# Kernel tuning notes

Hardware: AMD Instinct MI355X
Metric: run time of the kernel (lower is better)

Reference implementation:

```python
import jax, jax.numpy as jnp
import numpy as np

B_, C_, H_, W_, N_ = 2, 256, 64, 64, 16


def setup_inputs() -> dict:
    key = jax.random.key(0)
    ks = jax.random.split(key, 6)
    return {
        "features": jax.random.normal(ks[0], (B_, C_, H_, W_), jnp.float32),
        "A_log": jax.random.normal(ks[1], (C_, N_), jnp.float32) * 0.5,
        "D": jax.random.normal(ks[2], (C_,), jnp.float32),
        "W_delta": jax.random.normal(ks[3], (C_, C_), jnp.float32) * 0.02,
        "b_delta": jnp.zeros((C_,), jnp.float32),
        "W_B": jax.random.normal(ks[4], (C_, N_), jnp.float32) * 0.02,
        "W_C": jax.random.normal(ks[5], (C_, N_), jnp.float32) * 0.02,
    }


def _selective_scan(x, A_log, D, W_delta, b_delta, W_B, W_C):
    # x: (B, L, C) -> (B, L, C). Canonical S6 selective scan (mamba corrector).
    delta = jax.nn.softplus(x @ W_delta + b_delta)          # (B, L, C)
    Bm = x @ W_B                                            # (B, L, N)
    Cm = x @ W_C                                            # (B, L, N)
    A = -jnp.exp(A_log)                                     # (C, N), negative real
    dA = jnp.exp(delta[..., None] * A)                      # (B, L, C, N)
    dBx = (delta * x)[..., None] * Bm[:, :, None, :]        # (B, L, C, N)

    def combine(left, right):
        a_l, b_l = left
        a_r, b_r = right
        return (a_l * a_r, a_r * b_l + b_r)

    # h_t = dA_t * h_{t-1} + dBx_t, computed in parallel over L
    _, h = jax.lax.associative_scan(combine, (dA, dBx), axis=1)
    y = jnp.einsum('blcn,bln->blc', h, Cm) + x * D          # (B, L, C)
    return y


def reference(features, A_log, D, W_delta, b_delta, W_B, W_C):
    B, C, H, W = features.shape
    corr = lambda x: _selective_scan(x, A_log, D, W_delta, b_delta, W_B, W_C)

    # direction 1: row-major forward
    flat = features.reshape(B, C, H * W).transpose(0, 2, 1)        # (B, HW, C)
    out1 = corr(flat)
    # direction 2: row-major reversed
    out2 = jnp.flip(corr(jnp.flip(flat, axis=1)), axis=1)
    # direction 3: rows flipped vertically (flip over H), scan, flip back
    rows = features.transpose(0, 2, 3, 1)                          # (B, H, W, C)
    rows_f = jnp.flip(rows, axis=1).reshape(B, H * W, C)
    out3 = jnp.flip(corr(rows_f).reshape(B, H, W, C), axis=1).reshape(B, H * W, C)
    # direction 4: column-major, flipped over W, scan, flip + transpose back
    cols = features.transpose(0, 3, 2, 1)                          # (B, W, H, C)
    cols_f = jnp.flip(cols, axis=1).reshape(B, W * H, C)
    out4 = jnp.flip(corr(cols_f).reshape(B, W, H, C), axis=1)
    out4 = out4.transpose(0, 2, 1, 3).reshape(B, H * W, C)

    mamba_out = (out1 + out2 + out3 + out4) / 4                    # (B, HW, C)
    return mamba_out.transpose(0, 2, 1).reshape(B, C, H, W)
```

## Files before the change

### kernel.cpp

```cpp
#include <hip/hip_runtime.h>
#include <cstdint>
#include <cstddef>

#define BB 2
#define CC 256
#define NN 16
#define LL 4096
#define NCH 128
#define CLEN 32
#define LCH 16
#define LOG2E 1.4426950408889634f

__device__ __forceinline__ float softplus_f(float z) {
    return fmaxf(z, 0.f) + log1pf(expf(-fabsf(z)));
}

__global__ __launch_bounds__(256) void k1_delta_gemm(
    const float* __restrict__ feat, const float* __restrict__ Wd,
    const float* __restrict__ bd, const float* __restrict__ WB,
    const float* __restrict__ WC, float* __restrict__ du,
    float* __restrict__ Bm, float* __restrict__ Cm)
{
    int lc = blockIdx.x & 255;
    int b  = blockIdx.x >> 8;
    int l0 = lc * LCH;
    int c  = threadIdx.x;
    const float* fbase = feat + (size_t)b * CC * LL;

    int lB  = threadIdx.x >> 4;
    int s   = threadIdx.x & 15;
    int mat = s >> 3;
    int n0  = (s & 7) * 2;
    const float* wBC = mat ? WC : WB;

    float accM[LCH] = {};
    float accB0 = 0.f, accB1 = 0.f;

    #pragma unroll 4
    for (int k = 0; k < 256; ++k) {
        const float* frow = fbase + (size_t)k * LL + l0;
        float4 x0 = *(const float4*)(frow + 0);
        float4 x1 = *(const float4*)(frow + 4);
        float4 x2 = *(const float4*)(frow + 8);
        float4 x3 = *(const float4*)(frow + 12);
        float wv = Wd[(size_t)k * CC + c];
        float2 wb = *(const float2*)&wBC[k * NN + n0];
        float xb = frow[lB];

        accM[0]  = fmaf(x0.x, wv, accM[0]);
        accM[1]  = fmaf(x0.y, wv, accM[1]);
        accM[2]  = fmaf(x0.z, wv, accM[2]);
        accM[3]  = fmaf(x0.w, wv, accM[3]);
        accM[4]  = fmaf(x1.x, wv, accM[4]);
        accM[5]  = fmaf(x1.y, wv, accM[5]);
        accM[6]  = fmaf(x1.z, wv, accM[6]);
        accM[7]  = fmaf(x1.w, wv, accM[7]);
        accM[8]  = fmaf(x2.x, wv, accM[8]);
        accM[9]  = fmaf(x2.y, wv, accM[9]);
        accM[10] = fmaf(x2.z, wv, accM[10]);
        accM[11] = fmaf(x2.w, wv, accM[11]);
        accM[12] = fmaf(x3.x, wv, accM[12]);
        accM[13] = fmaf(x3.y, wv, accM[13]);
        accM[14] = fmaf(x3.z, wv, accM[14]);
        accM[15] = fmaf(x3.w, wv, accM[15]);
        accB0 = fmaf(xb, wb.x, accB0);
        accB1 = fmaf(xb, wb.y, accB1);
    }

    {
        float* dst = (mat ? Cm : Bm) + ((size_t)b * LL + l0 + lB) * NN + n0;
        *(float2*)dst = make_float2(accB0, accB1);
    }

    float bdc = bd[c];
    float4 fx[4];
    {
        const float* fcp = fbase + (size_t)c * LL + l0;
        fx[0] = *(const float4*)(fcp + 0);
        fx[1] = *(const float4*)(fcp + 4);
        fx[2] = *(const float4*)(fcp + 8);
        fx[3] = *(const float4*)(fcp + 12);
    }
    float2* du2 = (float2*)du;
    const float* fxs = (const float*)fx;
    #pragma unroll
    for (int j = 0; j < LCH; ++j) {
        float dv = softplus_f(accM[j] + bdc);
        float uv = dv * fxs[j];
        du2[((size_t)b * LL + l0 + j) * CC + c] = make_float2(dv, uv);
    }
}

__global__ __launch_bounds__(256, 4) void p1_aggr(
    const float2* __restrict__ du, const float* __restrict__ Bm,
    const float* __restrict__ A_log, float* __restrict__ P, float* __restrict__ S)
{
    int blk = blockIdx.x;
    int cls = blk >> 8;
    int b   = (blk >> 7) & 1;
    int ch  = blk & 127;
    int p0, inner;
    if (cls == 0)      { p0 = 32 * ch;        inner = 1; }
    else if (cls == 1) { p0 = 4095 - 32 * ch; inner = -1; }
    else               { p0 = 63 - (ch >> 1) + 2048 * (ch & 1); inner = 64; }
    int c = threadIdx.x;
    __shared__ float sBm[CLEN * NN];
    for (int i = threadIdx.x; i < CLEN * NN; i += 256) {
        int j = i >> 4, n = i & 15;
        sBm[i] = Bm[((size_t)b * LL + (p0 + inner * j)) * NN + n];
    }
    float A2[NN];
    {
        const float4* al = (const float4*)(A_log + c * NN);
        #pragma unroll
        for (int q = 0; q < 4; ++q) {
            float4 v = al[q];
            A2[q*4+0] = -expf(v.x) * LOG2E;
            A2[q*4+1] = -expf(v.y) * LOG2E;
            A2[q*4+2] = -expf(v.z) * LOG2E;
            A2[q*4+3] = -expf(v.w) * LOG2E;
        }
    }
    __syncthreads();
    float Sv[NN] = {};
    float sumd = 0.f;
    const float2* dub = du + (size_t)b * LL * CC + c;
    for (int j = 0; j < CLEN; ++j) {
        float2 dv = dub[(size_t)(p0 + inner * j) * CC];
        sumd += dv.x;
        float dA[NN];
        #pragma unroll
        for (int n = 0; n < NN; ++n) dA[n] = __builtin_amdgcn_exp2f(A2[n] * dv.x);
        #pragma unroll
        for (int n = 0; n < NN; ++n)
            Sv[n] = fmaf(dA[n], Sv[n], dv.y * sBm[j * 16 + n]);
    }
    size_t base = ((size_t)((cls * 2 + b) * 128 + ch)) * 4096 + (size_t)c * 16;
    #pragma unroll
    for (int n = 0; n < NN; ++n) {
        P[base + n] = __builtin_amdgcn_exp2f(A2[n] * sumd);
        S[base + n] = Sv[n];
    }
}

__global__ __launch_bounds__(128) void p2_scan(
    const float* __restrict__ P, const float* __restrict__ S, float* __restrict__ Hin)
{
    int r = blockIdx.x * 128 + threadIdx.x;
    int cn = r & 4095;
    int db = r >> 12;
    int d = db >> 1;
    int cls = (d == 1) ? 1 : ((d == 3) ? 2 : 0);
    int b = db & 1;
    const size_t cbase = ((size_t)(cls * 2 + b) * 128) * 4096 + cn;
    const size_t obase = ((size_t)db * 128) * 4096 + cn;
    float h = 0.f;
    for (int g = 0; g < 16; ++g) {
        float pv[8], sv[8];
        #pragma unroll
        for (int i = 0; i < 8; ++i) {
            int ch = g * 8 + i;
            int chm = (d == 2) ? (126 - 2 * (ch >> 1) + (ch & 1)) : ch;
            size_t ix = cbase + (size_t)chm * 4096;
            pv[i] = P[ix];
            sv[i] = S[ix];
        }
        #pragma unroll
        for (int i = 0; i < 8; ++i) {
            Hin[obase + (size_t)(g * 8 + i) * 4096] = h;
            h = fmaf(pv[i], h, sv[i]);
        }
    }
}

__global__ __launch_bounds__(256, 4) void p3_replay(
    const float2* __restrict__ du, const float* __restrict__ Bm,
    const float* __restrict__ Cm, const float* __restrict__ A_log,
    const float* __restrict__ Hin, float* __restrict__ yA,
    float* __restrict__ yB, float* __restrict__ yC)
{
    int blk = blockIdx.x;
    int sec = blk >> 8;
    int b   = (blk >> 7) & 1;
    int ch  = blk & 127;
    int p0, inner;
    if (sec == 0)      { p0 = 32 * ch;        inner = 1; }
    else if (sec == 1) { p0 = 4095 - 32 * ch; inner = -1; }
    else               { p0 = 63 - (ch >> 1) + 2048 * (ch & 1); inner = 64; }
    int c = threadIdx.x;
    __shared__ float sBm[CLEN * NN];
    __shared__ float sCm[CLEN * NN];
    for (int i = threadIdx.x; i < CLEN * NN; i += 256) {
        int j = i >> 4, n = i & 15;
        size_t o = ((size_t)b * LL + (p0 + inner * j)) * NN + n;
        sBm[i] = Bm[o];
        sCm[i] = Cm[o];
    }
    float A2[NN];
    {
        const float4* al = (const float4*)(A_log + c * NN);
        #pragma unroll
        for (int q = 0; q < 4; ++q) {
            float4 v = al[q];
            A2[q*4+0] = -expf(v.x) * LOG2E;
            A2[q*4+1] = -expf(v.y) * LOG2E;
            A2[q*4+2] = -expf(v.z) * LOG2E;
            A2[q*4+3] = -expf(v.w) * LOG2E;
        }
    }
    const float2* dub = du + (size_t)b * LL * CC + c;

    if (sec == 0) {
        int ch2 = 126 - (ch & ~1) + (ch & 1);
        float h0[NN], h2[NN];
        {
            const float4* hp0 = (const float4*)(Hin + ((size_t)(0 * 2 + b) * 128 + ch)  * 4096 + (size_t)c * 16);
            const float4* hp2 = (const float4*)(Hin + ((size_t)(2 * 2 + b) * 128 + ch2) * 4096 + (size_t)c * 16);
            #pragma unroll
            for (int q = 0; q < 4; ++q) {
                float4 v0 = hp0[q], v2 = hp2[q];
                h0[q*4+0]=v0.x; h0[q*4+1]=v0.y; h0[q*4+2]=v0.z; h0[q*4+3]=v0.w;
                h2[q*4+0]=v2.x; h2[q*4+1]=v2.y; h2[q*4+2]=v2.z; h2[q*4+3]=v2.w;
            }
        }
        __syncthreads();
        for (int j = 0; j < CLEN; ++j) {
            int p = p0 + j;
            float2 dv = dub[(size_t)p * CC];
            float dA[NN];
            #pragma unroll
            for (int n = 0; n < NN; ++n) dA[n] = __builtin_amdgcn_exp2f(A2[n] * dv.x);
            float y0v = 0.f, y2v = 0.f;
            #pragma unroll
            for (int n = 0; n < NN; ++n) {
                float Bu = dv.y * sBm[j * 16 + n];
                float cm = sCm[j * 16 + n];
                h0[n] = fmaf(dA[n], h0[n], Bu);
                h2[n] = fmaf(dA[n], h2[n], Bu);
                y0v = fmaf(h0[n], cm, y0v);
                y2v = fmaf(h2[n], cm, y2v);
            }
            yA[((size_t)b * LL + p) * CC + c] = 0.25f * (y0v + y2v);
        }
    } else {
        int d = (sec == 1) ? 1 : 3;
        float h[NN];
        {
            const float4* hp = (const float4*)(Hin + ((size_t)(d * 2 + b) * 128 + ch) * 4096 + (size_t)c * 16);
            #pragma unroll
            for (int q = 0; q < 4; ++q) {
                float4 v = hp[q];
                h[q*4+0]=v.x; h[q*4+1]=v.y; h[q*4+2]=v.z; h[q*4+3]=v.w;
            }
        }
        __syncthreads();
        float* yD = (sec == 1) ? yB : yC;
        for (int j = 0; j < CLEN; ++j) {
            int p = p0 + inner * j;
            float2 dv = dub[(size_t)p * CC];
            float dA[NN];
            #pragma unroll
            for (int n = 0; n < NN; ++n) dA[n] = __builtin_amdgcn_exp2f(A2[n] * dv.x);
            float yv = 0.f;
            #pragma unroll
            for (int n = 0; n < NN; ++n) {
                float Bu = dv.y * sBm[j * 16 + n];
                h[n] = fmaf(dA[n], h[n], Bu);
                yv = fmaf(h[n], sCm[j * 16 + n], yv);
            }
            yD[((size_t)b * LL + p) * CC + c] = 0.25f * yv;
        }
    }
}

__global__ __launch_bounds__(256) void k6_reduce(
    const float* __restrict__ feat, const float* __restrict__ D,
    const float* __restrict__ yA, const float* __restrict__ yB,
    const float* __restrict__ yC, float* __restrict__ out)
{
    int pt = blockIdx.x & 63;
    int ct = (blockIdx.x >> 6) & 3;
    int b  = blockIdx.x >> 8;
    int p0 = pt * 64, c0 = ct * 64;
    __shared__ float tile[64 * 65];
    {
        int cl = threadIdx.x & 63;
        int pg = threadIdx.x >> 6;
        #pragma unroll
        for (int pp = 0; pp < 16; ++pp) {
            int pl = pp * 4 + pg;
            size_t ix = ((size_t)b * LL + p0 + pl) * CC + c0 + cl;
            tile[cl * 65 + pl] = yA[ix] + yB[ix] + yC[ix];
        }
    }
    __syncthreads();
    {
        int pl = threadIdx.x & 63;
        int cg = threadIdx.x >> 6;
        #pragma unroll
        for (int cc = 0; cc < 16; ++cc) {
            int cloc = cc * 4 + cg;
            int c = c0 + cloc;
            size_t o = ((size_t)b * CC + c) * LL + p0 + pl;
            out[o] = tile[cloc * 65 + pl] + feat[o] * D[c];
        }
    }
}

extern "C" void kernel_launch(void* const* d_in, const int* in_sizes, int n_in,
                              void* d_out, int out_size, void* d_ws, size_t ws_size,
                              hipStream_t stream)
{
    const float* feat  = (const float*)d_in[0];
    const float* A_log = (const float*)d_in[1];
    const float* D     = (const float*)d_in[2];
    const float* Wd    = (const float*)d_in[3];
    const float* bd    = (const float*)d_in[4];
    const float* WB    = (const float*)d_in[5];
    const float* WC    = (const float*)d_in[6];
    float* out = (float*)d_out;

    float* ws  = (float*)d_ws;
    float* du  = ws;
    float* Bm  = du  + (size_t)4194304;
    float* Cm  = Bm  + (size_t)131072;
    float* P   = Cm  + (size_t)131072;
    float* S   = P   + (size_t)3145728;
    float* Hin = S   + (size_t)3145728;
    float* yA  = Hin + (size_t)4194304;
    float* yB  = yA  + (size_t)2097152;
    float* yC  = yB  + (size_t)2097152;

    k1_delta_gemm<<<512, 256, 0, stream>>>(feat, Wd, bd, WB, WC, du, Bm, Cm);
    p1_aggr<<<768, 256, 0, stream>>>((const float2*)du, Bm, A_log, P, S);
    p2_scan<<<256, 128, 0, stream>>>(P, S, Hin);
    p3_replay<<<768, 256, 0, stream>>>((const float2*)du, Bm, Cm, A_log, Hin, yA, yB, yC);
    k6_reduce<<<512, 256, 0, stream>>>(feat, D, yA, yB, yC, out);
}
```

Before: 177.6 us.

## Split state dimension across thread halves and halve GEMM token chunk

The delta GEMM kernel now processes 8 tokens per block instead of 16, doubling the grid to 1024 blocks, and computes one B/C output per thread. The aggregation and replay scan kernels now use 512 threads, with each channel's 16 state elements split across two threads of 8, halving per-thread registers and serial exp work. The replay kernel combines the two halves' partial outputs through shared-memory atomics into a 32x256 tile and then writes it out with coalesced float4 stores. This adds 32KB of shared memory per block, shared atomics and an extra barrier, and the GEMM reuses each loaded weight across fewer tokens.

```diff
diff --git a/kernel.cpp b/kernel.cpp
--- a/kernel.cpp
+++ b/kernel.cpp
@@ -8,7 +8,7 @@
 #define LL 4096
 #define NCH 128
 #define CLEN 32
-#define LCH 16
+#define LCH 8
 #define LOG2E 1.4426950408889634f
 
 __device__ __forceinline__ float softplus_f(float z) {
@@ -21,65 +21,49 @@
     const float* __restrict__ WC, float* __restrict__ du,
     float* __restrict__ Bm, float* __restrict__ Cm)
 {
-    int lc = blockIdx.x & 255;
-    int b  = blockIdx.x >> 8;
+    int lc = blockIdx.x & 511;
+    int b  = blockIdx.x >> 9;
     int l0 = lc * LCH;
     int c  = threadIdx.x;
     const float* fbase = feat + (size_t)b * CC * LL;
 
-    int lB  = threadIdx.x >> 4;
-    int s   = threadIdx.x & 15;
-    int mat = s >> 3;
-    int n0  = (s & 7) * 2;
+    int lB  = threadIdx.x >> 5;
+    int s   = threadIdx.x & 31;
+    int mat = s >> 4;
+    int n   = s & 15;
     const float* wBC = mat ? WC : WB;
 
     float accM[LCH] = {};
-    float accB0 = 0.f, accB1 = 0.f;
+    float accB = 0.f;
 
     #pragma unroll 4
     for (int k = 0; k < 256; ++k) {
         const float* frow = fbase + (size_t)k * LL + l0;
         float4 x0 = *(const float4*)(frow + 0);
         float4 x1 = *(const float4*)(frow + 4);
-        float4 x2 = *(const float4*)(frow + 8);
-        float4 x3 = *(const float4*)(frow + 12);
         float wv = Wd[(size_t)k * CC + c];
-        float2 wb = *(const float2*)&wBC[k * NN + n0];
+        float wb = wBC[k * NN + n];
         float xb = frow[lB];
 
-        accM[0]  = fmaf(x0.x, wv, accM[0]);
-        accM[1]  = fmaf(x0.y, wv, accM[1]);
-        accM[2]  = fmaf(x0.z, wv, accM[2]);
-        accM[3]  = fmaf(x0.w, wv, accM[3]);
-        accM[4]  = fmaf(x1.x, wv, accM[4]);
-        accM[5]  = fmaf(x1.y, wv, accM[5]);
-        accM[6]  = fmaf(x1.z, wv, accM[6]);
-        accM[7]  = fmaf(x1.w, wv, accM[7]);
-        accM[8]  = fmaf(x2.x, wv, accM[8]);
-        accM[9]  = fmaf(x2.y, wv, accM[9]);
-        accM[10] = fmaf(x2.z, wv, accM[10]);
-        accM[11] = fmaf(x2.w, wv, accM[11]);
-        accM[12] = fmaf(x3.x, wv, accM[12]);
-        accM[13] = fmaf(x3.y, wv, accM[13]);
-        accM[14] = fmaf(x3.z, wv, accM[14]);
-        accM[15] = fmaf(x3.w, wv, accM[15]);
-        accB0 = fmaf(xb, wb.x, accB0);
-        accB1 = fmaf(xb, wb.y, accB1);
-    }
-
-    {
-        float* dst = (mat ? Cm : Bm) + ((size_t)b * LL + l0 + lB) * NN + n0;
-        *(float2*)dst = make_float2(accB0, accB1);
-    }
+        accM[0] = fmaf(x0.x, wv, accM[0]);
+        accM[1] = fmaf(x0.y, wv, accM[1]);
+        accM[2] = fmaf(x0.z, wv, accM[2]);
+        accM[3] = fmaf(x0.w, wv, accM[3]);
+        accM[4] = fmaf(x1.x, wv, accM[4]);
+        accM[5] = fmaf(x1.y, wv, accM[5]);
+        accM[6] = fmaf(x1.z, wv, accM[6]);
+        accM[7] = fmaf(x1.w, wv, accM[7]);
+        accB = fmaf(xb, wb, accB);
+    }
+
+    (mat ? Cm : Bm)[((size_t)b * LL + l0 + lB) * NN + n] = accB;
 
     float bdc = bd[c];
-    float4 fx[4];
+    float4 fx[2];
     {
         const float* fcp = fbase + (size_t)c * LL + l0;
         fx[0] = *(const float4*)(fcp + 0);
         fx[1] = *(const float4*)(fcp + 4);
-        fx[2] = *(const float4*)(fcp + 8);
-        fx[3] = *(const float4*)(fcp + 12);
     }
     float2* du2 = (float2*)du;
     const float* fxs = (const float*)fx;
@@ -91,7 +75,7 @@
     }
 }
 
-__global__ __launch_bounds__(256, 4) void p1_aggr(
+__global__ __launch_bounds__(512) void p1_aggr(
     const float2* __restrict__ du, const float* __restrict__ Bm,
     const float* __restrict__ A_log, float* __restrict__ P, float* __restrict__ S)
 {
@@ -103,43 +87,42 @@
     if (cls == 0)      { p0 = 32 * ch;        inner = 1; }
     else if (cls == 1) { p0 = 4095 - 32 * ch; inner = -1; }
     else               { p0 = 63 - (ch >> 1) + 2048 * (ch & 1); inner = 64; }
-    int c = threadIdx.x;
+    int c  = threadIdx.x & 255;
+    int nh = threadIdx.x >> 8;
+    int n0 = nh * 8;
     __shared__ float sBm[CLEN * NN];
-    for (int i = threadIdx.x; i < CLEN * NN; i += 256) {
-        int j = i >> 4, n = i & 15;
-        sBm[i] = Bm[((size_t)b * LL + (p0 + inner * j)) * NN + n];
-    }
-    float A2[NN];
-    {
-        const float4* al = (const float4*)(A_log + c * NN);
-        #pragma unroll
-        for (int q = 0; q < 4; ++q) {
-            float4 v = al[q];
-            A2[q*4+0] = -expf(v.x) * LOG2E;
-            A2[q*4+1] = -expf(v.y) * LOG2E;
-            A2[q*4+2] = -expf(v.z) * LOG2E;
-            A2[q*4+3] = -expf(v.w) * LOG2E;
-        }
+    for (int i = threadIdx.x; i < CLEN * NN; i += 512) {
+        int j = i >> 4, nn = i & 15;
+        sBm[i] = Bm[((size_t)b * LL + (p0 + inner * j)) * NN + nn];
+    }
+    float A2[8];
+    {
+        const float4* al = (const float4*)(A_log + c * NN + n0);
+        float4 v0 = al[0], v1 = al[1];
+        A2[0] = -expf(v0.x) * LOG2E; A2[1] = -expf(v0.y) * LOG2E;
+        A2[2] = -expf(v0.z) * LOG2E; A2[3] = -expf(v0.w) * LOG2E;
+        A2[4] = -expf(v1.x) * LOG2E; A2[5] = -expf(v1.y) * LOG2E;
+        A2[6] = -expf(v1.z) * LOG2E; A2[7] = -expf(v1.w) * LOG2E;
     }
     __syncthreads();
-    float Sv[NN] = {};
+    float Sv[8] = {};
     float sumd = 0.f;
     const float2* dub = du + (size_t)b * LL * CC + c;
     for (int j = 0; j < CLEN; ++j) {
         float2 dv = dub[(size_t)(p0 + inner * j) * CC];
         sumd += dv.x;
-        float dA[NN];
-        #pragma unroll
-        for (int n = 0; n < NN; ++n) dA[n] = __builtin_amdgcn_exp2f(A2[n] * dv.x);
-        #pragma unroll
-        for (int n = 0; n < NN; ++n)
-            Sv[n] = fmaf(dA[n], Sv[n], dv.y * sBm[j * 16 + n]);
-    }
-    size_t base = ((size_t)((cls * 2 + b) * 128 + ch)) * 4096 + (size_t)c * 16;
+        float dA[8];
+        #pragma unroll
+        for (int i = 0; i < 8; ++i) dA[i] = __builtin_amdgcn_exp2f(A2[i] * dv.x);
+        #pragma unroll
+        for (int i = 0; i < 8; ++i)
+            Sv[i] = fmaf(dA[i], Sv[i], dv.y * sBm[j * 16 + n0 + i]);
+    }
+    size_t base = ((size_t)((cls * 2 + b) * 128 + ch)) * 4096 + (size_t)c * 16 + n0;
     #pragma unroll
-    for (int n = 0; n < NN; ++n) {
-        P[base + n] = __builtin_amdgcn_exp2f(A2[n] * sumd);
-        S[base + n] = Sv[n];
+    for (int i = 0; i < 8; ++i) {
+        P[base + i] = __builtin_amdgcn_exp2f(A2[i] * sumd);
+        S[base + i] = Sv[i];
     }
 }
 
@@ -173,7 +156,7 @@
     }
 }
 
-__global__ __launch_bounds__(256, 4) void p3_replay(
+__global__ __launch_bounds__(512) void p3_replay(
     const float2* __restrict__ du, const float* __restrict__ Bm,
     const float* __restrict__ Cm, const float* __restrict__ A_log,
     const float* __restrict__ Hin, float* __restrict__ yA,
@@ -187,90 +170,95 @@
     if (sec == 0)      { p0 = 32 * ch;        inner = 1; }
     else if (sec == 1) { p0 = 4095 - 32 * ch; inner = -1; }
     else               { p0 = 63 - (ch >> 1) + 2048 * (ch & 1); inner = 64; }
-    int c = threadIdx.x;
+    int c  = threadIdx.x & 255;
+    int nh = threadIdx.x >> 8;
+    int n0 = nh * 8;
     __shared__ float sBm[CLEN * NN];
     __shared__ float sCm[CLEN * NN];
-    for (int i = threadIdx.x; i < CLEN * NN; i += 256) {
-        int j = i >> 4, n = i & 15;
-        size_t o = ((size_t)b * LL + (p0 + inner * j)) * NN + n;
+    __shared__ float sY[CLEN * CC];
+    for (int i = threadIdx.x; i < CLEN * NN; i += 512) {
+        int j = i >> 4, nn = i & 15;
+        size_t o = ((size_t)b * LL + (p0 + inner * j)) * NN + nn;
         sBm[i] = Bm[o];
         sCm[i] = Cm[o];
     }
-    float A2[NN];
-    {
-        const float4* al = (const float4*)(A_log + c * NN);
-        #pragma unroll
-        for (int q = 0; q < 4; ++q) {
-            float4 v = al[q];
-            A2[q*4+0] = -expf(v.x) * LOG2E;
-            A2[q*4+1] = -expf(v.y) * LOG2E;
-            A2[q*4+2] = -expf(v.z) * LOG2E;
-            A2[q*4+3] = -expf(v.w) * LOG2E;
-        }
+    for (int i = threadIdx.x; i < CLEN * CC; i += 512) sY[i] = 0.f;
+    float A2[8];
+    {
+        const float4* al = (const float4*)(A_log + c * NN + n0);
+        float4 v0 = al[0], v1 = al[1];
+        A2[0] = -expf(v0.x) * LOG2E; A2[1] = -expf(v0.y) * LOG2E;
+        A2[2] = -expf(v0.z) * LOG2E; A2[3] = -expf(v0.w) * LOG2E;
+        A2[4] = -expf(v1.x) * LOG2E; A2[5] = -expf(v1.y) * LOG2E;
+        A2[6] = -expf(v1.z) * LOG2E; A2[7] = -expf(v1.w) * LOG2E;
     }
     const float2* dub = du + (size_t)b * LL * CC + c;
 
     if (sec == 0) {
         int ch2 = 126 - (ch & ~1) + (ch & 1);
-        float h0[NN], h2[NN];
+        float h0[8], h2[8];
         {
-            const float4* hp0 = (const float4*)(Hin + ((size_t)(0 * 2 + b) * 128 + ch)  * 4096 + (size_t)c * 16);
-            const float4* hp2 = (const float4*)(Hin + ((size_t)(2 * 2 + b) * 128 + ch2) * 4096 + (size_t)c * 16);
-            #pragma unroll
-            for (int q = 0; q < 4; ++q) {
-                float4 v0 = hp0[q], v2 = hp2[q];
-                h0[q*4+0]=v0.x; h0[q*4+1]=v0.y; h0[q*4+2]=v0.z; h0[q*4+3]=v0.w;
-                h2[q*4+0]=v2.x; h2[q*4+1]=v2.y; h2[q*4+2]=v2.z; h2[q*4+3]=v2.w;
-            }
+            const float4* hp0 = (const float4*)(Hin + ((size_t)(0 * 2 + b) * 128 + ch)  * 4096 + (size_t)c * 16 + n0);
+            const float4* hp2 = (const float4*)(Hin + ((size_t)(2 * 2 + b) * 128 + ch2) * 4096 + (size_t)c * 16 + n0);
+            float4 v0 = hp0[0], v1 = hp0[1], w0 = hp2[0], w1 = hp2[1];
+            h0[0]=v0.x; h0[1]=v0.y; h0[2]=v0.z; h0[3]=v0.w;
+            h0[4]=v1.x; h0[5]=v1.y; h0[6]=v1.z; h0[7]=v1.w;
+            h2[0]=w0.x; h2[1]=w0.y; h2[2]=w0.z; h2[3]=w0.w;
+            h2[4]=w1.x; h2[5]=w1.y; h2[6]=w1.z; h2[7]=w1.w;
         }
         __syncthreads();
         for (int j = 0; j < CLEN; ++j) {
-            int p = p0 + j;
-            float2 dv = dub[(size_t)p * CC];
-            float dA[NN];
+            float2 dv = dub[(size_t)(p0 + j) * CC];
+            float dA[8];
             #pragma unroll
-            for (int n = 0; n < NN; ++n) dA[n] = __builtin_amdgcn_exp2f(A2[n] * dv.x);
-            float y0v = 0.f, y2v = 0.f;
+            for (int i = 0; i < 8; ++i) dA[i] = __builtin_amdgcn_exp2f(A2[i] * dv.x);
+            float part = 0.f;
             #pragma unroll
-            for (int n = 0; n < NN; ++n) {
-                float Bu = dv.y * sBm[j * 16 + n];
-                float cm = sCm[j * 16 + n];
-                h0[n] = fmaf(dA[n], h0[n], Bu);
-                h2[n] = fmaf(dA[n], h2[n], Bu);
-                y0v = fmaf(h0[n], cm, y0v);
-                y2v = fmaf(h2[n], cm, y2v);
+            for (int i = 0; i < 8; ++i) {
+                float Bu = dv.y * sBm[j * 16 + n0 + i];
+                float cm = sCm[j * 16 + n0 + i];
+                h0[i] = fmaf(dA[i], h0[i], Bu);
+                h2[i] = fmaf(dA[i], h2[i], Bu);
+                part = fmaf(h0[i] + h2[i], cm, part);
             }
-            yA[((size_t)b * LL + p) * CC + c] = 0.25f * (y0v + y2v);
+            atomicAdd(&sY[j * CC + c], 0.25f * part);
         }
     } else {
         int d = (sec == 1) ? 1 : 3;
-        float h[NN];
+        float h[8];
         {
-            const float4* hp = (const float4*)(Hin + ((size_t)(d * 2 + b) * 128 + ch) * 4096 + (size_t)c * 16);
+            const float4* hp = (const float4*)(Hin + ((size_t)(d * 2 + b) * 128 + ch) * 4096 + (size_t)c * 16 + n0);
+            float4 v0 = hp[0], v1 = hp[1];
+            h[0]=v0.x; h[1]=v0.y; h[2]=v0.z; h[3]=v0.w;
+            h[4]=v1.x; h[5]=v1.y; h[6]=v1.z; h[7]=v1.w;
+        }
+        __syncthreads();
+        for (int j = 0; j < CLEN; ++j) {
+            float2 dv = dub[(size_t)(p0 + inner * j) * CC];
+            float dA[8];
             #pragma unroll
-            for (int q = 0; q < 4; ++q) {
-                float4 v = hp[q];
-                h[q*4+0]=v.x; h[q*4+1]=v.y; h[q*4+2]=v.z; h[q*4+3]=v.w;
+            for (int i = 0; i < 8; ++i) dA[i] = __builtin_amdgcn_exp2f(A2[i] * dv.x);
+            float part = 0.f;
+            #pragma unroll
+            for (int i = 0; i < 8; ++i) {
+                float Bu = dv.y * sBm[j * 16 + n0 + i];
+                h[i] = fmaf(dA[i], h[i], Bu);
+                part = fmaf(h[i], sCm[j * 16 + n0 + i], part);
             }
-        }
-        __syncthreads();
-        float* yD = (sec == 1) ? yB : yC;
-        for (int j = 0; j < CLEN; ++j) {
-            int p = p0 + inner * j;
-            float2 dv = dub[(size_t)p * CC];
-            float dA[NN];
-            #pragma unroll
-            for (int n = 0; n < NN; ++n) dA[n] = __builtin_amdgcn_exp2f(A2[n] * dv.x);
-            float yv = 0.f;
-            #pragma unroll
-            for (int n = 0; n < NN; ++n) {
-                float Bu = dv.y * sBm[j * 16 + n];
-                h[n] = fmaf(dA[n], h[n], Bu);
-                yv = fmaf(h[n], sCm[j * 16 + n], yv);
-            }
-            yD[((size_t)b * LL + p) * CC + c] = 0.25f * yv;
-        }
-    }
+            atomicAdd(&sY[j * CC + c], 0.25f * part);
+        }
+    }
+    __syncthreads();
+    float* yD = (sec == 0) ? yA : ((sec == 1) ? yB : yC);
+    int r   = threadIdx.x >> 4;
+    int cg  = (threadIdx.x & 15) * 16;
+    int jj  = (sec == 1) ? (31 - r) : r;
+    int tok = (sec == 2) ? (p0 + 64 * r) : ((sec == 1) ? (p0 - 31 + r) : (p0 + r));
+    float* gp = yD + ((size_t)b * LL + tok) * CC + cg;
+    const float* lp = &sY[jj * CC + cg];
+    #pragma unroll
+    for (int q = 0; q < 4; ++q)
+        *(float4*)(gp + q * 4) = *(const float4*)(lp + q * 4);
 }
 
 __global__ __launch_bounds__(256) void k6_reduce(
@@ -331,9 +319,9 @@
     float* yB  = yA  + (size_t)2097152;
     float* yC  = yB  + (size_t)2097152;
 
-    k1_delta_gemm<<<512, 256, 0, stream>>>(feat, Wd, bd, WB, WC, du, Bm, Cm);
-    p1_aggr<<<768, 256, 0, stream>>>((const float2*)du, Bm, A_log, P, S);
+    k1_delta_gemm<<<1024, 256, 0, stream>>>(feat, Wd, bd, WB, WC, du, Bm, Cm);
+    p1_aggr<<<768, 512, 0, stream>>>((const float2*)du, Bm, A_log, P, S);
     p2_scan<<<256, 128, 0, stream>>>(P, S, Hin);
-    p3_replay<<<768, 256, 0, stream>>>((const float2*)du, Bm, Cm, A_log, Hin, yA, yB, yC);
+    p3_replay<<<768, 512, 0, stream>>>((const float2*)du, Bm, Cm, A_log, Hin, yA, yB, yC);
     k6_reduce<<<512, 256, 0, stream>>>(feat, D, yA, yB, yC, out);
 }
```

New measurement: 223.5 us. +25.9%, slower.

## Double-buffer du loads in scan kernels and halve GEMM L-chunk

Applied to the files above, without the earlier changes.

The delta GEMM now processes 8 positions per block instead of 16, doubling the grid to 1024 blocks. Each thread computes one B/C output instead of two. The chunk scan (p1_aggr) and replay (p3_replay) loops are fully unrolled into groups of 8 with a double-buffered register prefetch of the du values, so global load latency overlaps the exp/FMA work. The occupancy hint of 4 is dropped from those launch bounds, giving the compiler room for the extra buffer registers at the possible cost of fewer waves per SIMD.

```diff
diff --git a/kernel.cpp b/kernel.cpp
--- a/kernel.cpp
+++ b/kernel.cpp
@@ -8,7 +8,7 @@
 #define LL 4096
 #define NCH 128
 #define CLEN 32
-#define LCH 16
+#define LCH 8
 #define LOG2E 1.4426950408889634f
 
 __device__ __forceinline__ float softplus_f(float z) {
@@ -21,65 +21,49 @@
     const float* __restrict__ WC, float* __restrict__ du,
     float* __restrict__ Bm, float* __restrict__ Cm)
 {
-    int lc = blockIdx.x & 255;
-    int b  = blockIdx.x >> 8;
+    int lc = blockIdx.x & 511;
+    int b  = blockIdx.x >> 9;
     int l0 = lc * LCH;
     int c  = threadIdx.x;
     const float* fbase = feat + (size_t)b * CC * LL;
 
-    int lB  = threadIdx.x >> 4;
-    int s   = threadIdx.x & 15;
-    int mat = s >> 3;
-    int n0  = (s & 7) * 2;
+    int lB  = threadIdx.x >> 5;
+    int s   = threadIdx.x & 31;
+    int mat = s >> 4;
+    int n   = s & 15;
     const float* wBC = mat ? WC : WB;
 
     float accM[LCH] = {};
-    float accB0 = 0.f, accB1 = 0.f;
+    float accB = 0.f;
 
     #pragma unroll 4
     for (int k = 0; k < 256; ++k) {
         const float* frow = fbase + (size_t)k * LL + l0;
         float4 x0 = *(const float4*)(frow + 0);
         float4 x1 = *(const float4*)(frow + 4);
-        float4 x2 = *(const float4*)(frow + 8);
-        float4 x3 = *(const float4*)(frow + 12);
         float wv = Wd[(size_t)k * CC + c];
-        float2 wb = *(const float2*)&wBC[k * NN + n0];
+        float wb = wBC[k * NN + n];
         float xb = frow[lB];
 
-        accM[0]  = fmaf(x0.x, wv, accM[0]);
-        accM[1]  = fmaf(x0.y, wv, accM[1]);
-        accM[2]  = fmaf(x0.z, wv, accM[2]);
-        accM[3]  = fmaf(x0.w, wv, accM[3]);
-        accM[4]  = fmaf(x1.x, wv, accM[4]);
-        accM[5]  = fmaf(x1.y, wv, accM[5]);
-        accM[6]  = fmaf(x1.z, wv, accM[6]);
-        accM[7]  = fmaf(x1.w, wv, accM[7]);
-        accM[8]  = fmaf(x2.x, wv, accM[8]);
-        accM[9]  = fmaf(x2.y, wv, accM[9]);
-        accM[10] = fmaf(x2.z, wv, accM[10]);
-        accM[11] = fmaf(x2.w, wv, accM[11]);
-        accM[12] = fmaf(x3.x, wv, accM[12]);
-        accM[13] = fmaf(x3.y, wv, accM[13]);
-        accM[14] = fmaf(x3.z, wv, accM[14]);
-        accM[15] = fmaf(x3.w, wv, accM[15]);
-        accB0 = fmaf(xb, wb.x, accB0);
-        accB1 = fmaf(xb, wb.y, accB1);
-    }
-
-    {
-        float* dst = (mat ? Cm : Bm) + ((size_t)b * LL + l0 + lB) * NN + n0;
-        *(float2*)dst = make_float2(accB0, accB1);
-    }
+        accM[0] = fmaf(x0.x, wv, accM[0]);
+        accM[1] = fmaf(x0.y, wv, accM[1]);
+        accM[2] = fmaf(x0.z, wv, accM[2]);
+        accM[3] = fmaf(x0.w, wv, accM[3]);
+        accM[4] = fmaf(x1.x, wv, accM[4]);
+        accM[5] = fmaf(x1.y, wv, accM[5]);
+        accM[6] = fmaf(x1.z, wv, accM[6]);
+        accM[7] = fmaf(x1.w, wv, accM[7]);
+        accB = fmaf(xb, wb, accB);
+    }
+
+    (mat ? Cm : Bm)[((size_t)b * LL + l0 + lB) * NN + n] = accB;
 
     float bdc = bd[c];
-    float4 fx[4];
+    float4 fx[2];
     {
         const float* fcp = fbase + (size_t)c * LL + l0;
         fx[0] = *(const float4*)(fcp + 0);
         fx[1] = *(const float4*)(fcp + 4);
-        fx[2] = *(const float4*)(fcp + 8);
-        fx[3] = *(const float4*)(fcp + 12);
     }
     float2* du2 = (float2*)du;
     const float* fxs = (const float*)fx;
@@ -91,7 +75,7 @@
     }
 }
 
-__global__ __launch_bounds__(256, 4) void p1_aggr(
+__global__ __launch_bounds__(256) void p1_aggr(
     const float2* __restrict__ du, const float* __restrict__ Bm,
     const float* __restrict__ A_log, float* __restrict__ P, float* __restrict__ S)
 {
@@ -106,8 +90,8 @@
     int c = threadIdx.x;
     __shared__ float sBm[CLEN * NN];
     for (int i = threadIdx.x; i < CLEN * NN; i += 256) {
-        int j = i >> 4, n = i & 15;
-        sBm[i] = Bm[((size_t)b * LL + (p0 + inner * j)) * NN + n];
+        int j = i >> 4, nn = i & 15;
+        sBm[i] = Bm[((size_t)b * LL + (p0 + inner * j)) * NN + nn];
     }
     float A2[NN];
     {
@@ -122,24 +106,38 @@
         }
     }
     __syncthreads();
+    const float2* dub = du + (size_t)b * LL * CC + c;
+    float2 buf[2][8];
+    #pragma unroll
+    for (int i = 0; i < 8; ++i)
+        buf[0][i] = dub[(size_t)(p0 + inner * i) * CC];
     float Sv[NN] = {};
     float sumd = 0.f;
-    const float2* dub = du + (size_t)b * LL * CC + c;
-    for (int j = 0; j < CLEN; ++j) {
-        float2 dv = dub[(size_t)(p0 + inner * j) * CC];
-        sumd += dv.x;
-        float dA[NN];
-        #pragma unroll
-        for (int n = 0; n < NN; ++n) dA[n] = __builtin_amdgcn_exp2f(A2[n] * dv.x);
-        #pragma unroll
-        for (int n = 0; n < NN; ++n)
-            Sv[n] = fmaf(dA[n], Sv[n], dv.y * sBm[j * 16 + n]);
+    #pragma unroll
+    for (int g = 0; g < 4; ++g) {
+        if (g < 3) {
+            #pragma unroll
+            for (int i = 0; i < 8; ++i)
+                buf[(g + 1) & 1][i] = dub[(size_t)(p0 + inner * ((g + 1) * 8 + i)) * CC];
+        }
+        #pragma unroll
+        for (int i = 0; i < 8; ++i) {
+            int j = g * 8 + i;
+            float2 dv = buf[g & 1][i];
+            sumd += dv.x;
+            float dA[NN];
+            #pragma unroll
+            for (int nn = 0; nn < NN; ++nn) dA[nn] = __builtin_amdgcn_exp2f(A2[nn] * dv.x);
+            #pragma unroll
+            for (int nn = 0; nn < NN; ++nn)
+                Sv[nn] = fmaf(dA[nn], Sv[nn], dv.y * sBm[j * 16 + nn]);
+        }
     }
     size_t base = ((size_t)((cls * 2 + b) * 128 + ch)) * 4096 + (size_t)c * 16;
     #pragma unroll
-    for (int n = 0; n < NN; ++n) {
-        P[base + n] = __builtin_amdgcn_exp2f(A2[n] * sumd);
-        S[base + n] = Sv[n];
+    for (int nn = 0; nn < NN; ++nn) {
+        P[base + nn] = __builtin_amdgcn_exp2f(A2[nn] * sumd);
+        S[base + nn] = Sv[nn];
     }
 }
 
@@ -173,7 +171,7 @@
     }
 }
 
-__global__ __launch_bounds__(256, 4) void p3_replay(
+__global__ __launch_bounds__(256) void p3_replay(
     const float2* __restrict__ du, const float* __restrict__ Bm,
     const float* __restrict__ Cm, const float* __restrict__ A_log,
     const float* __restrict__ Hin, float* __restrict__ yA,
@@ -191,8 +189,8 @@
     __shared__ float sBm[CLEN * NN];
     __shared__ float sCm[CLEN * NN];
     for (int i = threadIdx.x; i < CLEN * NN; i += 256) {
-        int j = i >> 4, n = i & 15;
-        size_t o = ((size_t)b * LL + (p0 + inner * j)) * NN + n;
+        int j = i >> 4, nn = i & 15;
+        size_t o = ((size_t)b * LL + (p0 + inner * j)) * NN + nn;
         sBm[i] = Bm[o];
         sCm[i] = Cm[o];
     }
@@ -224,23 +222,36 @@
             }
         }
         __syncthreads();
-        for (int j = 0; j < CLEN; ++j) {
-            int p = p0 + j;
-            float2 dv = dub[(size_t)p * CC];
-            float dA[NN];
-            #pragma unroll
-            for (int n = 0; n < NN; ++n) dA[n] = __builtin_amdgcn_exp2f(A2[n] * dv.x);
-            float y0v = 0.f, y2v = 0.f;
-            #pragma unroll
-            for (int n = 0; n < NN; ++n) {
-                float Bu = dv.y * sBm[j * 16 + n];
-                float cm = sCm[j * 16 + n];
-                h0[n] = fmaf(dA[n], h0[n], Bu);
-                h2[n] = fmaf(dA[n], h2[n], Bu);
-                y0v = fmaf(h0[n], cm, y0v);
-                y2v = fmaf(h2[n], cm, y2v);
-            }
-            yA[((size_t)b * LL + p) * CC + c] = 0.25f * (y0v + y2v);
+        float2 buf[2][8];
+        #pragma unroll
+        for (int i = 0; i < 8; ++i)
+            buf[0][i] = dub[(size_t)(p0 + i) * CC];
+        #pragma unroll
+        for (int g = 0; g < 4; ++g) {
+            if (g < 3) {
+                #pragma unroll
+                for (int i = 0; i < 8; ++i)
+                    buf[(g + 1) & 1][i] = dub[(size_t)(p0 + (g + 1) * 8 + i) * CC];
+            }
+            #pragma unroll
+            for (int i = 0; i < 8; ++i) {
+                int j = g * 8 + i;
+                float2 dv = buf[g & 1][i];
+                float dA[NN];
+                #pragma unroll
+                for (int nn = 0; nn < NN; ++nn) dA[nn] = __builtin_amdgcn_exp2f(A2[nn] * dv.x);
+                float y0v = 0.f, y2v = 0.f;
+                #pragma unroll
+                for (int nn = 0; nn < NN; ++nn) {
+                    float Bu = dv.y * sBm[j * 16 + nn];
+                    float cm = sCm[j * 16 + nn];
+                    h0[nn] = fmaf(dA[nn], h0[nn], Bu);
+                    h2[nn] = fmaf(dA[nn], h2[nn], Bu);
+                    y0v = fmaf(h0[nn], cm, y0v);
+                    y2v = fmaf(h2[nn], cm, y2v);
+                }
+                yA[((size_t)b * LL + p0 + j) * CC + c] = 0.25f * (y0v + y2v);
+            }
         }
     } else {
         int d = (sec == 1) ? 1 : 3;
@@ -255,20 +266,33 @@
         }
         __syncthreads();
         float* yD = (sec == 1) ? yB : yC;
-        for (int j = 0; j < CLEN; ++j) {
-            int p = p0 + inner * j;
-            float2 dv = dub[(size_t)p * CC];
-            float dA[NN];
-            #pragma unroll
-            for (int n = 0; n < NN; ++n) dA[n] = __builtin_amdgcn_exp2f(A2[n] * dv.x);
-            float yv = 0.f;
-            #pragma unroll
-            for (int n = 0; n < NN; ++n) {
-                float Bu = dv.y * sBm[j * 16 + n];
-                h[n] = fmaf(dA[n], h[n], Bu);
-                yv = fmaf(h[n], sCm[j * 16 + n], yv);
-            }
-            yD[((size_t)b * LL + p) * CC + c] = 0.25f * yv;
+        float2 buf[2][8];
+        #pragma unroll
+        for (int i = 0; i < 8; ++i)
+            buf[0][i] = dub[(size_t)(p0 + inner * i) * CC];
+        #pragma unroll
+        for (int g = 0; g < 4; ++g) {
+            if (g < 3) {
+                #pragma unroll
+                for (int i = 0; i < 8; ++i)
+                    buf[(g + 1) & 1][i] = dub[(size_t)(p0 + inner * ((g + 1) * 8 + i)) * CC];
+            }
+            #pragma unroll
+            for (int i = 0; i < 8; ++i) {
+                int j = g * 8 + i;
+                float2 dv = buf[g & 1][i];
+                float dA[NN];
+                #pragma unroll
+                for (int nn = 0; nn < NN; ++nn) dA[nn] = __builtin_amdgcn_exp2f(A2[nn] * dv.x);
+                float yv = 0.f;
+                #pragma unroll
+                for (int nn = 0; nn < NN; ++nn) {
+                    float Bu = dv.y * sBm[j * 16 + nn];
+                    h[nn] = fmaf(dA[nn], h[nn], Bu);
+                    yv = fmaf(h[nn], sCm[j * 16 + nn], yv);
+                }
+                yD[((size_t)b * LL + p0 + inner * j) * CC + c] = 0.25f * yv;
+            }
         }
     }
 }
@@ -331,7 +355,7 @@
     float* yB  = yA  + (size_t)2097152;
     float* yC  = yB  + (size_t)2097152;
 
-    k1_delta_gemm<<<512, 256, 0, stream>>>(feat, Wd, bd, WB, WC, du, Bm, Cm);
+    k1_delta_gemm<<<1024, 256, 0, stream>>>(feat, Wd, bd, WB, WC, du, Bm, Cm);
     p1_aggr<<<768, 256, 0, stream>>>((const float2*)du, Bm, A_log, P, S);
     p2_scan<<<256, 128, 0, stream>>>(P, S, Hin);
     p3_replay<<<768, 256, 0, stream>>>((const float2*)du, Bm, Cm, A_log, Hin, yA, yB, yC);
```

New measurement: 172.9 us. 1.03x faster.
